# Optimization experiments

Measured on AMD Instinct MI355X. Metric: run time of the kernel, lower is better.

Reference implementation:

```python
import jax, jax.numpy as jnp
import numpy as np

DEPTH, DIM, HEADS = 12, 768, 12
B, N = 2, 2048
HEAD_DIM = DIM // HEADS


def setup_inputs() -> dict:
    key = jax.random.key(0)
    ks = jax.random.split(key, 8)
    s = 0.02
    return {
        "x": jax.random.normal(ks[0], (B, N, DIM), jnp.float32),
        "sequence_ids": jnp.sort(jax.random.randint(ks[1], (B, N), 0, 8), axis=-1),
        "sequence_mask": jnp.zeros((B, N), dtype=bool),
        "ln1_w": jnp.ones((DEPTH, DIM), jnp.float32),
        "ln1_b": jnp.zeros((DEPTH, DIM), jnp.float32),
        "qkv_w": jax.random.normal(ks[2], (DEPTH, DIM, 3 * DIM), jnp.float32) * s,
        "qkv_b": jnp.zeros((DEPTH, 3 * DIM), jnp.float32),
        "proj_w": jax.random.normal(ks[3], (DEPTH, DIM, DIM), jnp.float32) * s,
        "proj_b": jnp.zeros((DEPTH, DIM), jnp.float32),
        "ls1_g": jnp.full((DEPTH, DIM), 1e-5, jnp.float32),
        "ln2_w": jnp.ones((DEPTH, DIM), jnp.float32),
        "ln2_b": jnp.zeros((DEPTH, DIM), jnp.float32),
        "fc1_w": jax.random.normal(ks[4], (DEPTH, DIM, 4 * DIM), jnp.float32) * s,
        "fc1_b": jnp.zeros((DEPTH, 4 * DIM), jnp.float32),
        "fc2_w": jax.random.normal(ks[5], (DEPTH, 4 * DIM, DIM), jnp.float32) * s,
        "fc2_b": jnp.zeros((DEPTH, DIM), jnp.float32),
        "ls2_g": jnp.full((DEPTH, DIM), 1e-5, jnp.float32),
        "r": 0,
    }


def _layernorm(x, w, b, eps=1e-5):
    m = x.mean(-1, keepdims=True)
    v = ((x - m) ** 2).mean(-1, keepdims=True)
    return (x - m) * jax.lax.rsqrt(v + eps) * w + b


def _attention(x, attn_mask, qkv_w, qkv_b, proj_w, proj_b):
    b, n, c = x.shape
    qkv = (x @ qkv_w + qkv_b).reshape(b, n, 3, HEADS, HEAD_DIM)
    qkv = jnp.transpose(qkv, (2, 0, 3, 1, 4))  # [3, B, H, N, hd]
    q, k, v = qkv[0], qkv[1], qkv[2]
    attn = jnp.einsum("bhqd,bhkd->bhqk", q, k) * (HEAD_DIM ** -0.5)
    neg_inf = jnp.finfo(attn.dtype).min
    attn = jnp.where(attn_mask[:, None, :, :], neg_inf, attn)  # broadcast over heads
    attn = jax.nn.softmax(attn, axis=-1)
    out = jnp.einsum("bhqk,bhkd->bhqd", attn, v)
    out = jnp.transpose(out, (0, 2, 1, 3)).reshape(b, n, c)
    return out @ proj_w + proj_b


def reference(x, sequence_ids, sequence_mask, ln1_w, ln1_b, qkv_w, qkv_b,
              proj_w, proj_b, ls1_g, ln2_w, ln2_b, fc1_w, fc1_b,
              fc2_w, fc2_b, ls2_g, r):
    # attn_mask: True where attention is NOT allowed
    attn_mask = sequence_ids[:, :, None] != sequence_ids[:, None, :]
    attn_mask = attn_mask | sequence_mask[:, :, None] | sequence_mask[:, None, :]
    for i in range(DEPTH):
        h = _layernorm(x, ln1_w[i], ln1_b[i])
        h = _attention(h, attn_mask, qkv_w[i], qkv_b[i], proj_w[i], proj_b[i])
        x = x + h * ls1_g[i]
        h = _layernorm(x, ln2_w[i], ln2_b[i])
        h = jax.nn.gelu(h @ fc1_w[i] + fc1_b[i], approximate=False) @ fc2_w[i] + fc2_b[i]
        x = x + h * ls2_g[i]
    return x
```

## Files before the change

kernel.cpp:

```cpp
#include <hip/hip_runtime.h>

#define NDEPTH 12
#define NDIM 768
#define NHEADS 12
#define NB 2
#define NSEQ 2048
#define MTOK (NB*NSEQ)

typedef short bf16x8 __attribute__((ext_vector_type(8)));
typedef float f32x4 __attribute__((ext_vector_type(4)));
typedef unsigned short u16;
typedef unsigned int u32;

#define L2E 1.44269504088896f

__device__ inline u16 f2bf(float f){
  union { float f; u32 u; } x; x.f = f;
  u32 r = x.u + 0x7fffu + ((x.u >> 16) & 1u);
  return (u16)(r >> 16);
}

__device__ inline f32x4 mfma16(bf16x8 a, bf16x8 b, f32x4 c){
  return __builtin_amdgcn_mfma_f32_16x16x32_bf16(a, b, c, 0, 0, 0);
}

#define GLOAD_LDS(gsrc, ldst) __builtin_amdgcn_global_load_lds( \
    (const __attribute__((address_space(1))) u32*)(gsrc), \
    (__attribute__((address_space(3))) u32*)(ldst), 16, 0, 0)

__device__ inline void ln_body(const float* __restrict__ x,
    const float* __restrict__ w, const float* __restrict__ b,
    u16* __restrict__ out, int blk){
  int wv = threadIdx.x >> 6, lane = threadIdx.x & 63;
  int row = blk * 4 + wv;
  const float* xr = x + (size_t)row * NDIM;
  float v[12];
  #pragma unroll
  for (int j = 0; j < 12; j++) v[j] = xr[lane + 64*j];
  float s = 0.f;
  #pragma unroll
  for (int j = 0; j < 12; j++) s += v[j];
  #pragma unroll
  for (int m = 1; m < 64; m <<= 1) s += __shfl_xor(s, m);
  float mean = s * (1.0f/768.0f);
  float q = 0.f;
  #pragma unroll
  for (int j = 0; j < 12; j++){ float d = v[j]-mean; q += d*d; }
  #pragma unroll
  for (int m = 1; m < 64; m <<= 1) q += __shfl_xor(q, m);
  float rs = rsqrtf(q * (1.0f/768.0f) + 1e-5f);
  u16* orow = out + (size_t)row * NDIM;
  #pragma unroll
  for (int j = 0; j < 12; j++){
    int c = lane + 64*j;
    orow[c] = f2bf((v[j]-mean)*rs*w[c] + b[c]);
  }
}

__global__ __launch_bounds__(256) void ln_kernel(const float* __restrict__ x,
    const float* __restrict__ w, const float* __restrict__ b,
    u16* __restrict__ out){
  ln_body(x, w, b, out, blockIdx.x);
}

__device__ inline void wtrans_body(const float* __restrict__ in,
    u16* __restrict__ out, int K, int N, int n0, int k0, float* tile){
  int t = threadIdx.x;
  #pragma unroll
  for (int j = 0; j < 16; j++){
    int idx = t + j*256;
    int r = idx >> 6, c = idx & 63;
    tile[r*65 + c] = in[(size_t)(k0+r)*N + n0 + c];
  }
  __syncthreads();
  #pragma unroll
  for (int j = 0; j < 16; j++){
    int idx = t + j*256;
    int c = idx >> 6, r = idx & 63;
    out[(size_t)(n0+c)*K + k0 + r] = f2bf(tile[r*65 + c]);
  }
}

__global__ __launch_bounds__(256) void lnwt_kernel(
    const float* __restrict__ x, const float* __restrict__ lw,
    const float* __restrict__ lb, u16* __restrict__ lout,
    const float* __restrict__ qkvw, const float* __restrict__ projw,
    const float* __restrict__ fc1w, const float* __restrict__ fc2w,
    u16* __restrict__ wq, u16* __restrict__ wp,
    u16* __restrict__ w1, u16* __restrict__ w2){
  __shared__ float tile[64*65];
  int bid = blockIdx.x;
  if (bid < 1024){ ln_body(x, lw, lb, lout, bid); return; }
  bid -= 1024;
  const float* in; u16* out; int K, N, tl;
  if (bid < 432){        in = qkvw; out = wq; K = 768;  N = 2304; tl = bid; }
  else if (bid < 576){   in = projw; out = wp; K = 768; N = 768;  tl = bid - 432; }
  else if (bid < 1152){  in = fc1w; out = w1; K = 768;  N = 3072; tl = bid - 576; }
  else {                 in = fc2w; out = w2; K = 3072; N = 768;  tl = bid - 1152; }
  int ntn = N >> 6;
  int n0 = (tl % ntn) << 6, k0 = (tl / ntn) << 6;
  wtrans_body(in, out, K, N, n0, k0, tile);
}

__global__ __launch_bounds__(256) void wtrans12_kernel(
    const float* __restrict__ qkvw, const float* __restrict__ projw,
    const float* __restrict__ fc1w, const float* __restrict__ fc2w,
    u16* __restrict__ wbase){
  __shared__ float tile[64*65];
  int bid = blockIdx.x;
  int layer = bid / 1728, sub = bid % 1728;
  u16* wl = wbase + (size_t)layer * 7077888;
  const float* in; u16* out; int K, N, tl;
  if (sub < 432){       in = qkvw + (size_t)layer*768*2304; out = wl;                 K = 768;  N = 2304; tl = sub; }
  else if (sub < 576){  in = projw + (size_t)layer*768*768; out = wl + 1769472;       K = 768;  N = 768;  tl = sub - 432; }
  else if (sub < 1152){ in = fc1w + (size_t)layer*768*3072; out = wl + 2359296;       K = 768;  N = 3072; tl = sub - 576; }
  else {                in = fc2w + (size_t)layer*3072*768; out = wl + 4718592;       K = 3072; N = 768;  tl = sub - 1152; }
  int ntn = N >> 6;
  int n0 = (tl % ntn) << 6, k0 = (tl / ntn) << 6;
  wtrans_body(in, out, K, N, n0, k0, tile);
}

template<int BN, int EPI>
__global__ __launch_bounds__(512) void gemm_kernel(
    const u16* __restrict__ A, const u16* __restrict__ Wt,
    const float* __restrict__ bias, const float* __restrict__ g,
    u16* __restrict__ outb, float* __restrict__ xres,
    int M, int N, int K)
{
  constexpr int WGN = BN / 32;
  constexpr int WGM = 8 / WGN;
  constexpr int WTM = 128 / WGM;
  constexpr int MI = WTM / 16;
  constexpr int NI = 2;
  __shared__ u16 As[2][128*64];
  __shared__ u16 Bs[2][BN*64];
  int nwg = gridDim.x;
  int bid = (blockIdx.x & 7) * (nwg >> 3) + (blockIdx.x >> 3);
  int nt = N / BN;
  int bm = bid / nt, bn = bid % nt;
  int m0 = bm*128, n0 = bn*BN;
  int t = threadIdx.x, lane = t & 63, wv = t >> 6;
  int wm = (wv / WGN) * WTM, wn = (wv % WGN) * 32;
  f32x4 acc[MI][NI] = {};
  int fr = lane & 15, fg = lane >> 4;

  auto stage = [&](int bf, int k0){
    #pragma unroll
    for (int i = 0; i < 2; i++){
      int off = t*16 + i*8192;
      int row = off >> 7, cb = off & 127;
      const char* src = (const char*)A + ((size_t)(m0+row)*K + k0)*2 + (cb ^ ((row&7)<<4));
      GLOAD_LDS(src, (char*)As[bf] + off);
    }
    #pragma unroll
    for (int i = 0; i < BN/64; i++){
      int off = t*16 + i*8192;
      int row = off >> 7, cb = off & 127;
      const char* src = (const char*)Wt + ((size_t)(n0+row)*K + k0)*2 + (cb ^ ((row&7)<<4));
      GLOAD_LDS(src, (char*)Bs[bf] + off);
    }
  };

  stage(0, 0);
  stage(1, 64);
  int cur = 0;
  int NS = K >> 6;
  for (int i = 0; i < NS; i++){
    if constexpr (BN == 128) asm volatile("s_waitcnt vmcnt(4)" ::: "memory");
    else                     asm volatile("s_waitcnt vmcnt(3)" ::: "memory");
    asm volatile("s_barrier" ::: "memory");

    bf16x8 af[MI][2], bfv[NI][2];
    #pragma unroll
    for (int mi = 0; mi < MI; mi++)
      #pragma unroll
      for (int kh = 0; kh < 2; kh++){
        int row = wm + mi*16 + fr;
        int off = (row*128 + kh*64 + fg*16) ^ ((row&7)<<4);
        af[mi][kh] = *(const bf16x8*)((const char*)As[cur] + off);
      }
    #pragma unroll
    for (int ni = 0; ni < NI; ni++)
      #pragma unroll
      for (int kh = 0; kh < 2; kh++){
        int row = wn + ni*16 + fr;
        int off = (row*128 + kh*64 + fg*16) ^ ((row&7)<<4);
        bfv[ni][kh] = *(const bf16x8*)((const char*)Bs[cur] + off);
      }
    #pragma unroll
    for (int mi = 0; mi < MI; mi++)
      #pragma unroll
      for (int ni = 0; ni < NI; ni++){
        acc[mi][ni] = mfma16(af[mi][0], bfv[ni][0], acc[mi][ni]);
        acc[mi][ni] = mfma16(af[mi][1], bfv[ni][1], acc[mi][ni]);
      }

    asm volatile("s_barrier" ::: "memory");
    if (i + 2 < NS) stage(cur, (i + 2) << 6);
    cur ^= 1;
  }

  int fq = fg << 2;
  #pragma unroll
  for (int mi = 0; mi < MI; mi++){
    #pragma unroll
    for (int ni = 0; ni < NI; ni++){
      int col = n0 + wn + ni*16 + fr;
      float bv = bias[col];
      #pragma unroll
      for (int r = 0; r < 4; r++){
        int row = m0 + wm + mi*16 + fq + r;
        float v = acc[mi][ni][r] + bv;
        if (EPI == 0){
          outb[(size_t)row * N + col] = f2bf(v);
        } else if (EPI == 1){
          float ge = 0.5f * v * (1.0f + erff(v * 0.70710678118f));
          outb[(size_t)row * N + col] = f2bf(ge);
        } else {
          xres[(size_t)row * N + col] += v * g[col];
        }
      }
    }
  }
}

__global__ __launch_bounds__(256) void attn_kernel(
    const u16* __restrict__ qkv, const int* __restrict__ sid,
    const unsigned char* __restrict__ smask, u16* __restrict__ outb)
{
  __shared__ u16 Ks[64][72];
  __shared__ u16 Vs[64][72];
  __shared__ u16 Ps[4][16][72];
  int nwg = gridDim.x;
  int blk = (blockIdx.x & 7) * (nwg >> 3) + (blockIdx.x >> 3);
  int qt = blk & 31; int bh = blk >> 5;
  int b = bh / NHEADS, h = bh % NHEADS;
  int t = threadIdx.x, lane = t & 63, wv = t >> 6;
  int q0 = qt << 6;
  size_t rowbase = (size_t)b * NSEQ;
  int fr = lane & 15, fg8 = (lane >> 4) << 3, fq = (lane >> 4) << 2;

  int qrow = q0 + (wv << 4) + fr;
  const u16* qp = qkv + (rowbase + qrow) * 2304 + h*64 + fg8;
  bf16x8 qf0 = *(const bf16x8*)qp;
  bf16x8 qf1 = *(const bf16x8*)(qp + 32);

  int qlo = sid[rowbase + q0];
  int qhi = sid[rowbase + q0 + 63];

  int sq[4]; int mq[4];
  #pragma unroll
  for (int r = 0; r < 4; r++){
    int qr = q0 + (wv << 4) + fq + r;
    sq[r] = sid[rowbase + qr];
    mq[r] = smask[rowbase + qr];
  }
  float m[4], l[4]; f32x4 o[4] = {};
  #pragma unroll
  for (int r = 0; r < 4; r++){ m[r] = -3.0e38f; l[r] = 0.f; }

  int skk = t >> 2, sd = (t & 3) << 4;

  for (int kt = 0; kt < NSEQ/64; kt++){
    int klo = sid[rowbase + (kt << 6)];
    int khi = sid[rowbase + (kt << 6) + 63];
    if (khi < qlo || klo > qhi) continue;

    __syncthreads();
    int krow = (kt << 6) + skk;
    const u16* kp = qkv + (rowbase + krow) * 2304 + 768 + h*64 + sd;
    *(uint4*)&Ks[skk][sd]     = *(const uint4*)kp;
    *(uint4*)&Ks[skk][sd + 8] = *(const uint4*)(kp + 8);
    const u16* vp = kp + 768;
    uint4 v0 = *(const uint4*)vp, v1 = *(const uint4*)(vp + 8);
    {
      const u16* vv = (const u16*)&v0;
      #pragma unroll
      for (int i = 0; i < 8; i++) Vs[sd + i][skk] = vv[i];
      vv = (const u16*)&v1;
      #pragma unroll
      for (int i = 0; i < 8; i++) Vs[sd + 8 + i][skk] = vv[i];
    }
    int ks[4]; int mk[4];
    #pragma unroll
    for (int s2 = 0; s2 < 4; s2++){
      int kk = (kt << 6) + (s2 << 4) + fr;
      ks[s2] = sid[rowbase + kk];
      mk[s2] = smask[rowbase + kk];
    }
    __syncthreads();

    f32x4 S[4];
    #pragma unroll
    for (int s2 = 0; s2 < 4; s2++){
      bf16x8 kf0 = *(const bf16x8*)&Ks[(s2 << 4) + fr][fg8];
      bf16x8 kf1 = *(const bf16x8*)&Ks[(s2 << 4) + fr][fg8 + 32];
      f32x4 s = {};
      s = mfma16(qf0, kf0, s);
      s = mfma16(qf1, kf1, s);
      #pragma unroll
      for (int r = 0; r < 4; r++){
        float v = s[r] * 0.125f;
        bool msk = (mq[r] | mk[s2]) || (sq[r] != ks[s2]);
        S[s2][r] = msk ? -3.0e38f : v;
      }
    }
    float mn[4], sf[4], rs[4];
    #pragma unroll
    for (int r = 0; r < 4; r++){
      float mx = fmaxf(fmaxf(S[0][r], S[1][r]), fmaxf(S[2][r], S[3][r]));
      #pragma unroll
      for (int d = 1; d < 16; d <<= 1) mx = fmaxf(mx, __shfl_xor(mx, d));
      mn[r] = fmaxf(m[r], mx);
      sf[r] = exp2f((m[r] - mn[r]) * L2E);
      rs[r] = 0.f;
    }
    #pragma unroll
    for (int s2 = 0; s2 < 4; s2++){
      #pragma unroll
      for (int r = 0; r < 4; r++){
        float p = exp2f((S[s2][r] - mn[r]) * L2E);
        rs[r] += p;
        Ps[wv][fq + r][(s2 << 4) + fr] = f2bf(p);
      }
    }
    #pragma unroll
    for (int r = 0; r < 4; r++){
      #pragma unroll
      for (int d = 1; d < 16; d <<= 1) rs[r] += __shfl_xor(rs[r], d);
      l[r] = l[r] * sf[r] + rs[r];
      m[r] = mn[r];
    }
    #pragma unroll
    for (int dsub = 0; dsub < 4; dsub++)
      #pragma unroll
      for (int r = 0; r < 4; r++) o[dsub][r] *= sf[r];
    __syncthreads();
    #pragma unroll
    for (int kg = 0; kg < 2; kg++){
      bf16x8 pf = *(const bf16x8*)&Ps[wv][fr][(kg << 5) + fg8];
      #pragma unroll
      for (int dsub = 0; dsub < 4; dsub++){
        bf16x8 vf = *(const bf16x8*)&Vs[(dsub << 4) + fr][(kg << 5) + fg8];
        o[dsub] = mfma16(pf, vf, o[dsub]);
      }
    }
  }

  #pragma unroll
  for (int dsub = 0; dsub < 4; dsub++){
    #pragma unroll
    for (int r = 0; r < 4; r++){
      int row = q0 + (wv << 4) + fq + r;
      int col = h*64 + (dsub << 4) + fr;
      outb[(rowbase + row) * NDIM + col] = f2bf(o[dsub][r] / l[r]);
    }
  }
}

extern "C" void kernel_launch(void* const* d_in, const int* in_sizes, int n_in,
                              void* d_out, int out_size, void* d_ws, size_t ws_size,
                              hipStream_t stream) {
  const float* x_in = (const float*)d_in[0];
  const int* sid = (const int*)d_in[1];
  const unsigned char* smask = (const unsigned char*)d_in[2];
  const float* ln1w = (const float*)d_in[3];
  const float* ln1b = (const float*)d_in[4];
  const float* qkvw = (const float*)d_in[5];
  const float* qkvb = (const float*)d_in[6];
  const float* projw = (const float*)d_in[7];
  const float* projb = (const float*)d_in[8];
  const float* ls1 = (const float*)d_in[9];
  const float* ln2w = (const float*)d_in[10];
  const float* ln2b = (const float*)d_in[11];
  const float* fc1w = (const float*)d_in[12];
  const float* fc1b = (const float*)d_in[13];
  const float* fc2w = (const float*)d_in[14];
  const float* fc2b = (const float*)d_in[15];
  const float* ls2 = (const float*)d_in[16];

  float* x = (float*)d_out;
  char* ws = (char*)d_ws;
  u16* hbuf   = (u16*)ws;
  u16* qkvbuf = (u16*)(ws + (size_t)6291456);
  u16* abuf   = (u16*)(ws + (size_t)25165824);
  u16* mbuf   = (u16*)(ws + (size_t)31457280);
  const size_t WT0 = 56623104;

  bool upfront  = ws_size >= (size_t)226492416;
  bool fused_wt = !upfront && ws_size >= WT0 + (size_t)14155776;
  u16* wall = (u16*)(ws + WT0);

  hipMemcpyAsync(x, x_in, (size_t)MTOK*NDIM*4, hipMemcpyDeviceToDevice, stream);

  if (upfront)
    wtrans12_kernel<<<12*1728, 256, 0, stream>>>(qkvw, projw, fc1w, fc2w, wall);

  for (int i = 0; i < NDEPTH; i++){
    const float* qw = qkvw + (size_t)i*NDIM*2304;
    const float* pw = projw + (size_t)i*NDIM*NDIM;
    const float* f1 = fc1w + (size_t)i*NDIM*3072;
    const float* f2 = fc2w + (size_t)i*3072*NDIM;

    u16 *wq, *wp, *w1, *w2;
    if (upfront){
      wq = wall + (size_t)i*7077888;
      wp = wq + 1769472; w1 = wp + 589824; w2 = w1 + 2359296;
    } else if (fused_wt){
      wq = wall; wp = wq + (size_t)2304*768;
      w1 = wp + (size_t)768*768; w2 = w1 + (size_t)768*3072;
    } else {
      wq = wp = w1 = w2 = wall;
    }

    if (fused_wt){
      lnwt_kernel<<<2752, 256, 0, stream>>>(x, ln1w + i*NDIM, ln1b + i*NDIM, hbuf,
                                            qw, pw, f1, f2, wq, wp, w1, w2);
    } else {
      ln_kernel<<<MTOK/4, 256, 0, stream>>>(x, ln1w + i*NDIM, ln1b + i*NDIM, hbuf);
    }
    gemm_kernel<128,0><<<(MTOK/128)*(2304/128), 512, 0, stream>>>(
        hbuf, wq, qkvb + (size_t)i*2304, nullptr, qkvbuf, nullptr, MTOK, 2304, NDIM);
    attn_kernel<<<NB*NHEADS*(NSEQ/64), 256, 0, stream>>>(qkvbuf, sid, smask, abuf);
    gemm_kernel<64,2><<<(MTOK/128)*(NDIM/64), 512, 0, stream>>>(
        abuf, wp, projb + (size_t)i*NDIM, ls1 + (size_t)i*NDIM,
        nullptr, x, MTOK, NDIM, NDIM);
    ln_kernel<<<MTOK/4, 256, 0, stream>>>(x, ln2w + i*NDIM, ln2b + i*NDIM, hbuf);
    gemm_kernel<128,1><<<(MTOK/128)*(3072/128), 512, 0, stream>>>(
        hbuf, w1, fc1b + (size_t)i*3072, nullptr, mbuf, nullptr, MTOK, 3072, NDIM);
    gemm_kernel<64,2><<<(MTOK/128)*(NDIM/64), 512, 0, stream>>>(
        mbuf, w2, fc2b + (size_t)i*NDIM, ls2 + (size_t)i*NDIM,
        nullptr, x, MTOK, NDIM, 3072);
  }
}
```

Before: 2.193 ms.

## Double-buffer attention K/V with a precomputed tile list and simplify GEMM prefetch

The attention kernel now builds a compact list of key tiles that share a sequence id with the query tile, using one wave's ballot. It double-buffers K in LDS through swizzled direct global-to-LDS loads and prefetches the next V tile and its mask data into registers while the current tile is computed. It also drops the block barrier before the P·V step, because each wave only reads its own P buffer. The GEMM main loop changes from staying two stages ahead with partial vmcnt waits to a simpler one-stage-ahead loop with __syncthreads, which may expose more load latency. The host weight-pointer selection is also restructured.

```diff
diff --git a/kernel.cpp b/kernel.cpp
--- a/kernel.cpp
+++ b/kernel.cpp
@@ -162,13 +162,10 @@
   };
 
   stage(0, 0);
-  stage(1, 64);
   int cur = 0;
-  int NS = K >> 6;
-  for (int i = 0; i < NS; i++){
-    if constexpr (BN == 128) asm volatile("s_waitcnt vmcnt(4)" ::: "memory");
-    else                     asm volatile("s_waitcnt vmcnt(3)" ::: "memory");
-    asm volatile("s_barrier" ::: "memory");
+  for (int k0 = 0; k0 < K; k0 += 64){
+    __syncthreads();
+    if (k0 + 64 < K) stage(cur ^ 1, k0 + 64);
 
     bf16x8 af[MI][2], bfv[NI][2];
     #pragma unroll
@@ -194,9 +191,6 @@
         acc[mi][ni] = mfma16(af[mi][0], bfv[ni][0], acc[mi][ni]);
         acc[mi][ni] = mfma16(af[mi][1], bfv[ni][1], acc[mi][ni]);
       }
-
-    asm volatile("s_barrier" ::: "memory");
-    if (i + 2 < NS) stage(cur, (i + 2) << 6);
     cur ^= 1;
   }
 
@@ -228,9 +222,10 @@
     const u16* __restrict__ qkv, const int* __restrict__ sid,
     const unsigned char* __restrict__ smask, u16* __restrict__ outb)
 {
-  __shared__ u16 Ks[64][72];
-  __shared__ u16 Vs[64][72];
+  __shared__ u16 Ks[2][4096];
+  __shared__ u16 Vs[2][64][72];
   __shared__ u16 Ps[4][16][72];
+  __shared__ int tl[33];
   int nwg = gridDim.x;
   int blk = (blockIdx.x & 7) * (nwg >> 3) + (blockIdx.x >> 3);
   int qt = blk & 31; int bh = blk >> 5;
@@ -238,7 +233,7 @@
   int t = threadIdx.x, lane = t & 63, wv = t >> 6;
   int q0 = qt << 6;
   size_t rowbase = (size_t)b * NSEQ;
-  int fr = lane & 15, fg8 = (lane >> 4) << 3, fq = (lane >> 4) << 2;
+  int fr = lane & 15, fg = lane >> 4, fg8 = fg << 3, fq = fg << 2;
 
   int qrow = q0 + (wv << 4) + fr;
   const u16* qp = qkv + (rowbase + qrow) * 2304 + h*64 + fg8;
@@ -248,6 +243,18 @@
   int qlo = sid[rowbase + q0];
   int qhi = sid[rowbase + q0 + 63];
 
+  if (wv == 0){
+    bool al = false;
+    if (lane < 32){
+      int klo = sid[rowbase + (lane << 6)];
+      int khi = sid[rowbase + (lane << 6) + 63];
+      al = (khi >= qlo) && (klo <= qhi);
+    }
+    unsigned long long bal = __ballot(al);
+    if (al) tl[__popcll(bal & ((1ull << lane) - 1ull))] = lane;
+    if (lane == 0) tl[32] = __popcll(bal);
+  }
+
   int sq[4]; int mq[4];
   #pragma unroll
   for (int r = 0; r < 4; r++){
@@ -261,47 +268,79 @@
 
   int skk = t >> 2, sd = (t & 3) << 4;
 
-  for (int kt = 0; kt < NSEQ/64; kt++){
-    int klo = sid[rowbase + (kt << 6)];
-    int khi = sid[rowbase + (kt << 6) + 63];
-    if (khi < qlo || klo > qhi) continue;
-
-    __syncthreads();
-    int krow = (kt << 6) + skk;
-    const u16* kp = qkv + (rowbase + krow) * 2304 + 768 + h*64 + sd;
-    *(uint4*)&Ks[skk][sd]     = *(const uint4*)kp;
-    *(uint4*)&Ks[skk][sd + 8] = *(const uint4*)(kp + 8);
-    const u16* vp = kp + 768;
-    uint4 v0 = *(const uint4*)vp, v1 = *(const uint4*)(vp + 8);
+  __syncthreads();
+  int tcnt = tl[32];
+
+  auto stageK = [&](int bf, int tile){
+    #pragma unroll
+    for (int i = 0; i < 2; i++){
+      int off = t*16 + i*4096;
+      int row = off >> 7, cb = off & 127;
+      const char* src = (const char*)(qkv + (rowbase + (tile<<6) + row)*2304 + 768 + h*64)
+                        + (cb ^ ((row&7)<<4));
+      GLOAD_LDS(src, (char*)&Ks[bf][0] + off);
+    }
+  };
+
+  int tcur = tl[0];
+  uint4 v0c, v1c;
+  {
+    const u16* vp = qkv + (rowbase + (tcur<<6) + skk) * 2304 + 1536 + h*64 + sd;
+    v0c = *(const uint4*)vp; v1c = *(const uint4*)(vp + 8);
+  }
+  stageK(0, tcur);
+  int ksc[4], mkc[4];
+  #pragma unroll
+  for (int s2 = 0; s2 < 4; s2++){
+    int kk = (tcur << 6) + (s2 << 4) + fr;
+    ksc[s2] = sid[rowbase + kk];
+    mkc[s2] = smask[rowbase + kk];
+  }
+
+  for (int j = 0; j < tcnt; j++){
+    int cur = j & 1;
+    asm volatile("s_waitcnt vmcnt(0)" ::: "memory");
     {
-      const u16* vv = (const u16*)&v0;
-      #pragma unroll
-      for (int i = 0; i < 8; i++) Vs[sd + i][skk] = vv[i];
-      vv = (const u16*)&v1;
-      #pragma unroll
-      for (int i = 0; i < 8; i++) Vs[sd + 8 + i][skk] = vv[i];
-    }
-    int ks[4]; int mk[4];
+      const u16* vv = (const u16*)&v0c;
+      #pragma unroll
+      for (int i = 0; i < 8; i++) Vs[cur][sd + i][skk] = vv[i];
+      vv = (const u16*)&v1c;
+      #pragma unroll
+      for (int i = 0; i < 8; i++) Vs[cur][sd + 8 + i][skk] = vv[i];
+    }
+    bool hasnext = (j + 1 < tcnt);
+    int tnext = hasnext ? tl[j + 1] : tcur;
+    uint4 v0n = v0c, v1n = v1c; int ksn[4], mkn[4];
+    #pragma unroll
+    for (int s2 = 0; s2 < 4; s2++){ ksn[s2] = ksc[s2]; mkn[s2] = mkc[s2]; }
+    if (hasnext){
+      const u16* vp = qkv + (rowbase + (tnext<<6) + skk) * 2304 + 1536 + h*64 + sd;
+      v0n = *(const uint4*)vp; v1n = *(const uint4*)(vp + 8);
+      #pragma unroll
+      for (int s2 = 0; s2 < 4; s2++){
+        int kk = (tnext << 6) + (s2 << 4) + fr;
+        ksn[s2] = sid[rowbase + kk];
+        mkn[s2] = smask[rowbase + kk];
+      }
+    }
+    asm volatile("s_waitcnt lgkmcnt(0)" ::: "memory");
+    asm volatile("s_barrier" ::: "memory");
+    if (hasnext) stageK(cur ^ 1, tnext);
+
+    f32x4 S[4];
     #pragma unroll
     for (int s2 = 0; s2 < 4; s2++){
-      int kk = (kt << 6) + (s2 << 4) + fr;
-      ks[s2] = sid[rowbase + kk];
-      mk[s2] = smask[rowbase + kk];
-    }
-    __syncthreads();
-
-    f32x4 S[4];
-    #pragma unroll
-    for (int s2 = 0; s2 < 4; s2++){
-      bf16x8 kf0 = *(const bf16x8*)&Ks[(s2 << 4) + fr][fg8];
-      bf16x8 kf1 = *(const bf16x8*)&Ks[(s2 << 4) + fr][fg8 + 32];
+      int row = (s2 << 4) + fr;
+      int ob = (row*128 + fg*16) ^ ((row&7)<<4);
+      bf16x8 kf0 = *(const bf16x8*)((const char*)&Ks[cur][0] + ob);
+      bf16x8 kf1 = *(const bf16x8*)((const char*)&Ks[cur][0] + (ob ^ 64));
       f32x4 s = {};
       s = mfma16(qf0, kf0, s);
       s = mfma16(qf1, kf1, s);
       #pragma unroll
       for (int r = 0; r < 4; r++){
         float v = s[r] * 0.125f;
-        bool msk = (mq[r] | mk[s2]) || (sq[r] != ks[s2]);
+        bool msk = (mq[r] | mkc[s2]) || (sq[r] != ksc[s2]);
         S[s2][r] = msk ? -3.0e38f : v;
       }
     }
@@ -335,16 +374,19 @@
     for (int dsub = 0; dsub < 4; dsub++)
       #pragma unroll
       for (int r = 0; r < 4; r++) o[dsub][r] *= sf[r];
-    __syncthreads();
+    asm volatile("s_waitcnt lgkmcnt(0)" ::: "memory");
     #pragma unroll
     for (int kg = 0; kg < 2; kg++){
       bf16x8 pf = *(const bf16x8*)&Ps[wv][fr][(kg << 5) + fg8];
       #pragma unroll
       for (int dsub = 0; dsub < 4; dsub++){
-        bf16x8 vf = *(const bf16x8*)&Vs[(dsub << 4) + fr][(kg << 5) + fg8];
+        bf16x8 vf = *(const bf16x8*)&Vs[cur][(dsub << 4) + fr][(kg << 5) + fg8];
         o[dsub] = mfma16(pf, vf, o[dsub]);
       }
     }
+    v0c = v0n; v1c = v1n; tcur = tnext;
+    #pragma unroll
+    for (int s2 = 0; s2 < 4; s2++){ ksc[s2] = ksn[s2]; mkc[s2] = mkn[s2]; }
   }
 
   #pragma unroll
@@ -406,14 +448,12 @@
     if (upfront){
       wq = wall + (size_t)i*7077888;
       wp = wq + 1769472; w1 = wp + 589824; w2 = w1 + 2359296;
-    } else if (fused_wt){
+    } else {
       wq = wall; wp = wq + (size_t)2304*768;
       w1 = wp + (size_t)768*768; w2 = w1 + (size_t)768*3072;
-    } else {
-      wq = wp = w1 = w2 = wall;
-    }
-
-    if (fused_wt){
+    }
+
+    if (!upfront && fused_wt){
       lnwt_kernel<<<2752, 256, 0, stream>>>(x, ln1w + i*NDIM, ln1b + i*NDIM, hbuf,
                                             qw, pw, f1, f2, wq, wp, w1, w2);
     } else {
```

After: 2.238 ms. +2.1%, slower.
